# Kernel optimization log

Measured on AMD Instinct MI355X. Metric: run time of the kernel, lower is better.

The kernel has to match this reference:

```python
import jax, jax.numpy as jnp
import numpy as np
from math import factorial

# ---- module hyperparameters (from init_kwargs) ----
SPECIES = np.array([1, 6, 7, 8], np.int32)
LOW, HIGH, NG, RSWITCH, W, LMAX = 0.0, 6.0, 20, 1.0, 2.0, 2
LWEIGHTS = np.array([1.0, 1.0, 1.0], np.float32)
INVF = [2.0, 2.0, 2.0]


def _angular_tables():
    comps, weights, idx, inv = [], [], [], []
    for i in range(LMAX + 1):
        for k in range(i + 1):
            for m in range(i - k + 1):
                n = i - k - m
                comps.append([n, m, k])
                weights.append(factorial(i) / (factorial(n) * factorial(m) * factorial(k)))
                idx.append(i)
                inv.append(INVF[i])
    return (np.array(comps, np.int32), np.array(weights, np.float32),
            np.array(idx, np.int32), np.array(inv, np.float32))

COMPS, ANGW, ANGIDX, INVFACT = _angular_tables()   # 10 angular components for lmax=2
OFFSETS = np.linspace(LOW, HIGH, NG + 1, dtype=np.float32)[1:]
SQRTPI = np.float32(np.sqrt(np.pi))
NSP = len(SPECIES)
COMBOS = [(i, j) for i in range(NSP) for j in range(i + 1, NSP)]
NMBODY = NSP + len(COMBOS)
FPSIZE = NG * (LMAX + 1) * NMBODY


def _int_pow(x, e):
    # e in {0,1,2}; avoids NaN from pow(negative_base, float_exponent)
    return jnp.where(e == 0, jnp.ones_like(x), jnp.where(e == 1, x, x * x))


def _forward(coordinates, nuclear_charges, natom_counts, neighbours):
    B, N, _ = coordinates.shape
    mask = neighbours >= 0                              # padded slots are -1
    nb = jnp.maximum(neighbours, 0)                     # safe_fill
    bidx = jnp.arange(B)[:, None, None]
    local = coordinates[bidx, nb]                       # [B,N,M,3] neighbour gather
    nbh = coordinates[:, :, None, :] - local
    nbh = jnp.where(mask[..., None], nbh, 1.0)          # keep padded slots finite
    d = jnp.linalg.norm(nbh, axis=3)                    # [B,N,M]
    coeff = mask.astype(coordinates.dtype)
    nbr_z = nuclear_charges[bidx, nb]                   # [B,N,M]

    dsw = (d - RSWITCH) / (HIGH - RSWITCH)
    cut = 1.0 - 6.0 * dsw**5 + 15.0 * dsw**4 - 10.0 * dsw**3
    d2 = d * d
    sigma2 = jnp.log(1.0 + W / d2)
    mu = jnp.log(d / jnp.sqrt(1.0 + W / d2))
    off = jnp.asarray(OFFSETS)
    centered = (jnp.log(off) - mu[..., None]) ** 2      # [B,N,M,G]
    s2 = sigma2[..., None]
    radial = (1.0 / (off * jnp.sqrt(s2) * SQRTPI)) * jnp.exp(-centered / (2.0 * s2)) \
             * cut[..., None] * coeff[..., None]        # [B,N,M,G]

    expo = jnp.asarray(INVFACT + ANGIDX.astype(np.float32))
    inv_scaling = (1.0 / d[..., None]) ** expo * coeff[..., None]   # [B,N,M,A]
    comps = jnp.asarray(COMPS)
    angular = inv_scaling \
        * _int_pow(nbh[..., None, 0], comps[:, 0]) \
        * _int_pow(nbh[..., None, 1], comps[:, 1]) \
        * _int_pow(nbh[..., None, 2], comps[:, 2])      # [B,N,M,A]

    angw = jnp.asarray(ANGW)
    lw = jnp.asarray(LWEIGHTS)
    onehot = jnp.asarray((ANGIDX[:, None] == np.arange(LMAX + 1)[None, :]).astype(np.float32))

    sp_masks = [(nbr_z == int(z)).astype(coordinates.dtype) for z in SPECIES]

    def group_fp(gmask):
        ang = angular * gmask[..., None]
        t = jnp.einsum('bnma,bnmg->bnag', ang, radial)          # sum over neighbours
        orb = angw[None, None, :, None] * (t * t)               # [B,N,A,G]
        elem = jnp.einsum('bnag,al->bnlg', orb, onehot)         # index_add over l
        return lw[None, None, :, None] * elem                   # [B,N,L+1,G]

    fps = [group_fp(m) for m in sp_masks]
    for (i, j) in COMBOS:
        gmask = jnp.maximum(sp_masks[i], sp_masks[j])
        fps.append(group_fp(gmask) - (fps[i] + fps[j]))

    fp = jnp.stack(fps, axis=3)                                 # [B,N,L+1,NMBODY,G]
    atom_mask = (jnp.arange(N)[None, :] < natom_counts[:, None]).astype(coordinates.dtype)
    fp = fp * atom_mask[:, :, None, None, None]
    return fp.reshape(B, N, FPSIZE)


def setup_inputs() -> dict:
    rng = np.random.default_rng(0)
    B, N, M = 128, 128, 64
    box = 13.5
    coords = rng.uniform(0.0, box, (B, N, 3)).astype(np.float32)
    charges = rng.choice(np.array([1, 6, 7, 8], np.int32), size=(B, N)).astype(np.int32)
    counts = rng.integers(96, N + 1, B).astype(np.int32)
    diff = coords[:, :, None, :] - coords[:, None, :, :]
    dist = np.linalg.norm(diff, axis=-1)
    exist = np.arange(N)[None, :] < counts[:, None]
    valid = (dist < HIGH) & (dist > 1e-6) & exist[:, :, None] & exist[:, None, :]
    order = np.argsort(~valid, axis=2, kind='stable')[:, :, :M]
    vmask = np.take_along_axis(valid, order, axis=2)
    neighbours = np.where(vmask, order, -1).astype(np.int32)
    return {
        "coordinates": jnp.asarray(coords),
        "nuclear_charges": jnp.asarray(charges),
        "natom_counts": jnp.asarray(counts),
        "neighbours": jnp.asarray(neighbours),
    }


def reference(coordinates, nuclear_charges, natom_counts, neighbours):
    return _forward(coordinates, nuclear_charges, natom_counts, neighbours)
```

## Files before the change

### kernel.cpp

```cpp
#include <hip/hip_runtime.h>


#define B_   128
#define N_   128
#define M_   64
#define NG_  20
#define NSP_ 4
#define FPSIZE_ 600
#define APB  16
#define BLOCK_THREADS (APB * NG_)
#define NWAVE (BLOCK_THREADS / 64)
#define P1ITER ((APB + NWAVE - 1) / NWAVE)

__global__ __launch_bounds__(BLOCK_THREADS, 5)
void gto_fp_kernel(const float* __restrict__ coords,
                   const int*   __restrict__ charges,
                   const int*   __restrict__ counts,
                   const int*   __restrict__ neigh,
                   float*       __restrict__ out)
{
    __shared__ float4 sP[APB][M_ + 1];
    __shared__ float2 sQ[APB][M_ + 1];
    __shared__ int    s_seg[APB][NSP_ + 1];

    const int tid  = threadIdx.x;
    const int lane = tid & 63;
    const int wid  = tid >> 6;
    const int blockBase = blockIdx.x * APB;
    const int bidx = blockBase / N_;

#pragma unroll
    for (int it = 0; it < P1ITER; ++it) {
        const int la = wid + it * NWAVE;
        if (la < APB) {
            const int atom = blockBase + la;
            const int nb = neigh[atom * M_ + lane];
            bool v = (nb >= 0);
            int s = 0;
            float4 P = make_float4(0.f, 0.f, 0.f, 0.f);
            float2 Q = make_float2(0.f, 0.f);
            if (v) {
                const int nidx = bidx * N_ + nb;
                const float dx = coords[atom * 3 + 0] - coords[nidx * 3 + 0];
                const float dy = coords[atom * 3 + 1] - coords[nidx * 3 + 1];
                const float dz = coords[atom * 3 + 2] - coords[nidx * 3 + 2];
                const int   z  = charges[nidx];

                const float d2     = dx * dx + dy * dy + dz * dz;
                const float inv_d  = __builtin_amdgcn_rsqf(d2);
                const float d      = d2 * inv_d;
                const float inv_d2 = inv_d * inv_d;

                const float dsw  = (d - 1.0f) * 0.2f;
                const float dsw2 = dsw * dsw;
                const float cut  = 1.0f - dsw2 * dsw * fmaf(6.0f, dsw2, fmaf(-15.0f, dsw, 10.0f));

                const float sigma2 = __logf(fmaf(2.0f, inv_d2, 1.0f));
                const float mu     = 0.5f * (__logf(d2) - sigma2);
                const float amp    = fmaxf(__builtin_amdgcn_rsqf(sigma2) * cut * inv_d2,
                                           1.0e-30f);

                const float F  = -0.72134752f * __builtin_amdgcn_rcpf(sigma2);
                const float Fm = F * mu;
                const float c0 = F;
                const float c1 = -(Fm + Fm);
                const float c2 = fmaf(Fm, mu, __log2f(amp));

                s = (z == 1) ? 0 : (z - 5);
                P = make_float4(c0, c1, c2, dx * inv_d);
                Q = make_float2(dy * inv_d, dz * inv_d);
            }
            const unsigned long long b0 = __ballot(v && (s == 0));
            const unsigned long long b1 = __ballot(v && (s == 1));
            const unsigned long long b2 = __ballot(v && (s == 2));
            const unsigned long long b3 = __ballot(v && (s == 3));
            const int c0n = __popcll(b0), c1n = __popcll(b1),
                      c2n = __popcll(b2), c3n = __popcll(b3);
            const int o0 = __builtin_amdgcn_mbcnt_hi((unsigned)(b0 >> 32),
                           __builtin_amdgcn_mbcnt_lo((unsigned)b0, 0u));
            const int o1 = __builtin_amdgcn_mbcnt_hi((unsigned)(b1 >> 32),
                           __builtin_amdgcn_mbcnt_lo((unsigned)b1, 0u));
            const int o2 = __builtin_amdgcn_mbcnt_hi((unsigned)(b2 >> 32),
                           __builtin_amdgcn_mbcnt_lo((unsigned)b2, 0u));
            const int o3 = __builtin_amdgcn_mbcnt_hi((unsigned)(b3 >> 32),
                           __builtin_amdgcn_mbcnt_lo((unsigned)b3, 0u));
            int slot = o0;
            slot = (s == 1) ? c0n + o1 : slot;
            slot = (s == 2) ? c0n + c1n + o2 : slot;
            slot = (s == 3) ? c0n + c1n + c2n + o3 : slot;
            if (v) {
                sP[la][slot] = P;
                sQ[la][slot] = Q;
            }
            if (lane == 0) {
                s_seg[la][0] = 0;
                s_seg[la][1] = c0n;
                s_seg[la][2] = c0n + c1n;
                s_seg[la][3] = c0n + c1n + c2n;
                s_seg[la][4] = c0n + c1n + c2n + c3n;
            }
        }
    }
    __syncthreads();

    const int g  = tid % NG_;
    const int la = tid / NG_;
    const int atom = blockBase + la;
    const int n = atom % N_;

    const float off         = 0.3f * (float)(g + 1);
    const float lo          = __logf(off);
    const float lo2         = lo * lo;
    const float inv_off_spi = 1.0f / (off * 1.7724538509055159f);

    float T[NSP_][10];
#pragma unroll
    for (int s = 0; s < NSP_; ++s)
#pragma unroll
        for (int a = 0; a < 10; ++a) T[s][a] = 0.0f;

#define BODY(SS, P, Q)                                                        \
    {                                                                         \
        const float rad = __builtin_amdgcn_exp2f(                             \
            fmaf(P.x, lo2, fmaf(P.y, lo, P.z)));                              \
        const float rx = rad * P.w, ry = rad * Q.x, rz = rad * Q.y;           \
        T[SS][0] += rad;                                                      \
        T[SS][1] += rx;  T[SS][2] += ry;  T[SS][3] += rz;                     \
        T[SS][4] = fmaf(rx, P.w, T[SS][4]);                                   \
        T[SS][5] = fmaf(rx, Q.x, T[SS][5]);                                   \
        T[SS][6] = fmaf(ry, Q.x, T[SS][6]);                                   \
        T[SS][7] = fmaf(rx, Q.y, T[SS][7]);                                   \
        T[SS][8] = fmaf(ry, Q.y, T[SS][8]);                                   \
        T[SS][9] = fmaf(rz, Q.y, T[SS][9]);                                   \
    }

#define ACC(SS)                                                               \
    {                                                                         \
        const int e0 = s_seg[la][SS];                                         \
        const int e1 = s_seg[la][SS + 1];                                     \
        int m = e0;                                                           \
        for (; m + 3 < e1; m += 4) {                                          \
            const float4 Pa = sP[la][m];     const float2 Qa = sQ[la][m];     \
            const float4 Pb = sP[la][m + 1]; const float2 Qb = sQ[la][m + 1]; \
            const float4 Pc = sP[la][m + 2]; const float2 Qc = sQ[la][m + 2]; \
            const float4 Pd = sP[la][m + 3]; const float2 Qd = sQ[la][m + 3]; \
            BODY(SS, Pa, Qa)                                                  \
            BODY(SS, Pb, Qb)                                                  \
            BODY(SS, Pc, Qc)                                                  \
            BODY(SS, Pd, Qd)                                                  \
        }                                                                     \
        for (; m < e1; ++m) {                                                 \
            const float4 Pa = sP[la][m]; const float2 Qa = sQ[la][m];         \
            BODY(SS, Pa, Qa)                                                  \
        }                                                                     \
    }
    ACC(0) ACC(1) ACC(2) ACC(3)
#undef ACC
#undef BODY

    const float amask = (n < counts[bidx]) ? 1.0f : 0.0f;
    const float scale = amask * inv_off_spi * inv_off_spi;
    float* op = out + atom * FPSIZE_ + g;

#pragma unroll
    for (int l = 0; l < 3; ++l) {
        const int a0 = (l == 0) ? 0 : (l == 1) ? 1 : 4;
        const int a1 = (l == 0) ? 1 : (l == 1) ? 4 : 10;
#pragma unroll
        for (int s = 0; s < NSP_; ++s) {
            float v = 0.0f;
#pragma unroll
            for (int a = a0; a < a1; ++a) {
                const float w = (a == 5 || a == 7 || a == 8) ? 2.0f : 1.0f;
                v = fmaf(w * T[s][a], T[s][a], v);
            }
            op[(l * 10 + s) * NG_] = scale * v;
        }
        int mb = 4;
#pragma unroll
        for (int i = 0; i < NSP_; ++i) {
#pragma unroll
            for (int j = i + 1; j < NSP_; ++j) {
                float v = 0.0f;
#pragma unroll
                for (int a = a0; a < a1; ++a) {
                    const float w = (a == 5 || a == 7 || a == 8) ? 2.0f : 1.0f;
                    v = fmaf(w * T[i][a], T[j][a], v);
                }
                op[(l * 10 + mb) * NG_] = scale * (2.0f * v);
                ++mb;
            }
        }
    }
}

extern "C" void kernel_launch(void* const* d_in, const int* in_sizes, int n_in,
                              void* d_out, int out_size, void* d_ws, size_t ws_size,
                              hipStream_t stream) {
    const float* coords  = (const float*)d_in[0];
    const int*   charges = (const int*)d_in[1];
    const int*   counts  = (const int*)d_in[2];
    const int*   neigh   = (const int*)d_in[3];
    float*       outp    = (float*)d_out;

    const int blocks = (B_ * N_) / APB;
    gto_fp_kernel<<<blocks, BLOCK_THREADS, 0, stream>>>(coords, charges, counts, neigh, outp);
}
```

Before: 88.19 us.

## Compute two Gaussians per thread and stage molecule coords/charges in LDS

Each thread now handles two radial Gaussian offsets, g and g+10, instead of one. This halves the number of times each neighbour's P/Q entries are read from LDS and raises instruction-level parallelism. Blocks now cover 32 atoms with 10 threads each. The whole molecule's coordinates and species indices are first copied into shared memory, so the neighbour gather reads LDS instead of global memory. The costs are roughly double the accumulator registers (80 floats), more LDS per block, and dropping the occupancy hint from the launch bounds.

Result: no change. 88.48 us (+0.3%).

```diff
diff --git a/kernel.cpp b/kernel.cpp
--- a/kernel.cpp
+++ b/kernel.cpp
@@ -7,12 +7,13 @@
 #define NG_  20
 #define NSP_ 4
 #define FPSIZE_ 600
-#define APB  16
-#define BLOCK_THREADS (APB * NG_)
+#define APB  32
+#define TPA  10
+#define BLOCK_THREADS (APB * TPA)
 #define NWAVE (BLOCK_THREADS / 64)
 #define P1ITER ((APB + NWAVE - 1) / NWAVE)
 
-__global__ __launch_bounds__(BLOCK_THREADS, 5)
+__global__ __launch_bounds__(BLOCK_THREADS)
 void gto_fp_kernel(const float* __restrict__ coords,
                    const int*   __restrict__ charges,
                    const int*   __restrict__ counts,
@@ -21,30 +22,44 @@
 {
     __shared__ float4 sP[APB][M_ + 1];
     __shared__ float2 sQ[APB][M_ + 1];
+    __shared__ float  sC[3 * N_];
+    __shared__ int    sZ[N_];
     __shared__ int    s_seg[APB][NSP_ + 1];
 
     const int tid  = threadIdx.x;
     const int lane = tid & 63;
     const int wid  = tid >> 6;
     const int blockBase = blockIdx.x * APB;
-    const int bidx = blockBase / N_;
+    const int bidx      = blockBase / N_;
+    const int alocBase  = blockBase - bidx * N_;
+
+    for (int i = tid; i < 3 * N_; i += BLOCK_THREADS)
+        sC[i] = coords[bidx * 3 * N_ + i];
+    for (int i = tid; i < N_; i += BLOCK_THREADS) {
+        const int z = charges[bidx * N_ + i];
+        sZ[i] = (z == 1) ? 0 : (z - 5);
+    }
+    __syncthreads();
 
 #pragma unroll
     for (int it = 0; it < P1ITER; ++it) {
         const int la = wid + it * NWAVE;
         if (la < APB) {
             const int atom = blockBase + la;
+            const int aloc = alocBase + la;
             const int nb = neigh[atom * M_ + lane];
             bool v = (nb >= 0);
             int s = 0;
             float4 P = make_float4(0.f, 0.f, 0.f, 0.f);
             float2 Q = make_float2(0.f, 0.f);
             if (v) {
-                const int nidx = bidx * N_ + nb;
-                const float dx = coords[atom * 3 + 0] - coords[nidx * 3 + 0];
-                const float dy = coords[atom * 3 + 1] - coords[nidx * 3 + 1];
-                const float dz = coords[atom * 3 + 2] - coords[nidx * 3 + 2];
-                const int   z  = charges[nidx];
+                const float ax = sC[aloc * 3 + 0];
+                const float ay = sC[aloc * 3 + 1];
+                const float az = sC[aloc * 3 + 2];
+                const float dx = ax - sC[nb * 3 + 0];
+                const float dy = ay - sC[nb * 3 + 1];
+                const float dz = az - sC[nb * 3 + 2];
+                s = sZ[nb];
 
                 const float d2     = dx * dx + dy * dy + dz * dz;
                 const float inv_d  = __builtin_amdgcn_rsqf(d2);
@@ -66,7 +81,6 @@
                 const float c1 = -(Fm + Fm);
                 const float c2 = fmaf(Fm, mu, __log2f(amp));
 
-                s = (z == 1) ? 0 : (z - 5);
                 P = make_float4(c0, c1, c2, dx * inv_d);
                 Q = make_float2(dy * inv_d, dz * inv_d);
             }
@@ -103,35 +117,46 @@
     }
     __syncthreads();
 
-    const int g  = tid % NG_;
-    const int la = tid / NG_;
+    const int g0 = tid % TPA;
+    const int la = tid / TPA;
     const int atom = blockBase + la;
-    const int n = atom % N_;
-
-    const float off         = 0.3f * (float)(g + 1);
-    const float lo          = __logf(off);
-    const float lo2         = lo * lo;
-    const float inv_off_spi = 1.0f / (off * 1.7724538509055159f);
-
-    float T[NSP_][10];
+    const int aloc = alocBase + la;
+
+    const float offA = 0.3f * (float)(g0 + 1);
+    const float offB = 0.3f * (float)(g0 + 11);
+    const float loA = __logf(offA), loA2 = loA * loA;
+    const float loB = __logf(offB), loB2 = loB * loB;
+
+    float TA[NSP_][10], TB[NSP_][10];
 #pragma unroll
     for (int s = 0; s < NSP_; ++s)
 #pragma unroll
-        for (int a = 0; a < 10; ++a) T[s][a] = 0.0f;
+        for (int a = 0; a < 10; ++a) { TA[s][a] = 0.0f; TB[s][a] = 0.0f; }
 
 #define BODY(SS, P, Q)                                                        \
     {                                                                         \
-        const float rad = __builtin_amdgcn_exp2f(                             \
-            fmaf(P.x, lo2, fmaf(P.y, lo, P.z)));                              \
-        const float rx = rad * P.w, ry = rad * Q.x, rz = rad * Q.y;           \
-        T[SS][0] += rad;                                                      \
-        T[SS][1] += rx;  T[SS][2] += ry;  T[SS][3] += rz;                     \
-        T[SS][4] = fmaf(rx, P.w, T[SS][4]);                                   \
-        T[SS][5] = fmaf(rx, Q.x, T[SS][5]);                                   \
-        T[SS][6] = fmaf(ry, Q.x, T[SS][6]);                                   \
-        T[SS][7] = fmaf(rx, Q.y, T[SS][7]);                                   \
-        T[SS][8] = fmaf(ry, Q.y, T[SS][8]);                                   \
-        T[SS][9] = fmaf(rz, Q.y, T[SS][9]);                                   \
+        const float radA = __builtin_amdgcn_exp2f(                            \
+            fmaf(P.x, loA2, fmaf(P.y, loA, P.z)));                            \
+        const float radB = __builtin_amdgcn_exp2f(                            \
+            fmaf(P.x, loB2, fmaf(P.y, loB, P.z)));                            \
+        const float rxA = radA * P.w, ryA = radA * Q.x, rzA = radA * Q.y;     \
+        const float rxB = radB * P.w, ryB = radB * Q.x, rzB = radB * Q.y;     \
+        TA[SS][0] += radA;                 TB[SS][0] += radB;                 \
+        TA[SS][1] += rxA;                  TB[SS][1] += rxB;                  \
+        TA[SS][2] += ryA;                  TB[SS][2] += ryB;                  \
+        TA[SS][3] += rzA;                  TB[SS][3] += rzB;                  \
+        TA[SS][4] = fmaf(rxA, P.w, TA[SS][4]);                                \
+        TA[SS][5] = fmaf(rxA, Q.x, TA[SS][5]);                                \
+        TA[SS][6] = fmaf(ryA, Q.x, TA[SS][6]);                                \
+        TA[SS][7] = fmaf(rxA, Q.y, TA[SS][7]);                                \
+        TA[SS][8] = fmaf(ryA, Q.y, TA[SS][8]);                                \
+        TA[SS][9] = fmaf(rzA, Q.y, TA[SS][9]);                                \
+        TB[SS][4] = fmaf(rxB, P.w, TB[SS][4]);                                \
+        TB[SS][5] = fmaf(rxB, Q.x, TB[SS][5]);                                \
+        TB[SS][6] = fmaf(ryB, Q.x, TB[SS][6]);                                \
+        TB[SS][7] = fmaf(rxB, Q.y, TB[SS][7]);                                \
+        TB[SS][8] = fmaf(ryB, Q.y, TB[SS][8]);                                \
+        TB[SS][9] = fmaf(rzB, Q.y, TB[SS][9]);                                \
     }
 
 #define ACC(SS)                                                               \
@@ -139,17 +164,13 @@
         const int e0 = s_seg[la][SS];                                         \
         const int e1 = s_seg[la][SS + 1];                                     \
         int m = e0;                                                           \
-        for (; m + 3 < e1; m += 4) {                                          \
+        for (; m + 1 < e1; m += 2) {                                          \
             const float4 Pa = sP[la][m];     const float2 Qa = sQ[la][m];     \
             const float4 Pb = sP[la][m + 1]; const float2 Qb = sQ[la][m + 1]; \
-            const float4 Pc = sP[la][m + 2]; const float2 Qc = sQ[la][m + 2]; \
-            const float4 Pd = sP[la][m + 3]; const float2 Qd = sQ[la][m + 3]; \
             BODY(SS, Pa, Qa)                                                  \
             BODY(SS, Pb, Qb)                                                  \
-            BODY(SS, Pc, Qc)                                                  \
-            BODY(SS, Pd, Qd)                                                  \
         }                                                                     \
-        for (; m < e1; ++m) {                                                 \
+        if (m < e1) {                                                         \
             const float4 Pa = sP[la][m]; const float2 Qa = sQ[la][m];         \
             BODY(SS, Pa, Qa)                                                  \
         }                                                                     \
@@ -158,40 +179,45 @@
 #undef ACC
 #undef BODY
 
-    const float amask = (n < counts[bidx]) ? 1.0f : 0.0f;
-    const float scale = amask * inv_off_spi * inv_off_spi;
-    float* op = out + atom * FPSIZE_ + g;
-
-#pragma unroll
-    for (int l = 0; l < 3; ++l) {
-        const int a0 = (l == 0) ? 0 : (l == 1) ? 1 : 4;
-        const int a1 = (l == 0) ? 1 : (l == 1) ? 4 : 10;
-#pragma unroll
-        for (int s = 0; s < NSP_; ++s) {
-            float v = 0.0f;
-#pragma unroll
-            for (int a = a0; a < a1; ++a) {
-                const float w = (a == 5 || a == 7 || a == 8) ? 2.0f : 1.0f;
-                v = fmaf(w * T[s][a], T[s][a], v);
-            }
-            op[(l * 10 + s) * NG_] = scale * v;
-        }
-        int mb = 4;
-#pragma unroll
-        for (int i = 0; i < NSP_; ++i) {
-#pragma unroll
-            for (int j = i + 1; j < NSP_; ++j) {
+    const float amask = (aloc < counts[bidx]) ? 1.0f : 0.0f;
+
+    auto epilogue = [&](const float (&T)[NSP_][10], const int g, const float off) {
+        const float iosp  = 1.0f / (off * 1.7724538509055159f);
+        const float scale = amask * iosp * iosp;
+        float* op = out + atom * FPSIZE_ + g;
+#pragma unroll
+        for (int l = 0; l < 3; ++l) {
+            const int a0 = (l == 0) ? 0 : (l == 1) ? 1 : 4;
+            const int a1 = (l == 0) ? 1 : (l == 1) ? 4 : 10;
+#pragma unroll
+            for (int s = 0; s < NSP_; ++s) {
                 float v = 0.0f;
 #pragma unroll
                 for (int a = a0; a < a1; ++a) {
                     const float w = (a == 5 || a == 7 || a == 8) ? 2.0f : 1.0f;
-                    v = fmaf(w * T[i][a], T[j][a], v);
+                    v = fmaf(w * T[s][a], T[s][a], v);
                 }
-                op[(l * 10 + mb) * NG_] = scale * (2.0f * v);
-                ++mb;
+                op[(l * 10 + s) * NG_] = scale * v;
+            }
+            int mb = 4;
+#pragma unroll
+            for (int i = 0; i < NSP_; ++i) {
+#pragma unroll
+                for (int j = i + 1; j < NSP_; ++j) {
+                    float v = 0.0f;
+#pragma unroll
+                    for (int a = a0; a < a1; ++a) {
+                        const float w = (a == 5 || a == 7 || a == 8) ? 2.0f : 1.0f;
+                        v = fmaf(w * T[i][a], T[j][a], v);
+                    }
+                    op[(l * 10 + mb) * NG_] = scale * (2.0f * v);
+                    ++mb;
+                }
             }
         }
-    }
+    };
+    epilogue(TA, g0, offA);
+    epilogue(TB, g0 + 10, offB);
 }
 
 extern "C" void kernel_launch(void* const* d_in, const int* in_sizes, int n_in,
```

## Stage molecule coordinates in LDS, pair-store outputs, unroll tail, drop occupancy hint

Applied to the files above, without the earlier changes.

Each block now stages the whole molecule's coordinates and species indices into shared memory, so neighbour lookups read LDS instead of scattered global loads. Output stores are widened to float2 by exchanging values between adjacent lanes with a shuffle, so only even lanes write. The tail loop of the accumulation is unrolled into fixed 2+1 steps, and the min-blocks-per-CU launch bound is removed. This adds an extra barrier and LDS footprint per block, and the float2 stores rely on each lane pair sitting in the same wave and on 8-byte alignment.

After: 85.46 us. 3.1% less time.

```diff
diff --git a/kernel.cpp b/kernel.cpp
--- a/kernel.cpp
+++ b/kernel.cpp
@@ -8,11 +8,12 @@
 #define NSP_ 4
 #define FPSIZE_ 600
 #define APB  16
-#define BLOCK_THREADS (APB * NG_)
+#define TPA  20
+#define BLOCK_THREADS (APB * TPA)
 #define NWAVE (BLOCK_THREADS / 64)
 #define P1ITER ((APB + NWAVE - 1) / NWAVE)
 
-__global__ __launch_bounds__(BLOCK_THREADS, 5)
+__global__ __launch_bounds__(BLOCK_THREADS)
 void gto_fp_kernel(const float* __restrict__ coords,
                    const int*   __restrict__ charges,
                    const int*   __restrict__ counts,
@@ -21,30 +22,44 @@
 {
     __shared__ float4 sP[APB][M_ + 1];
     __shared__ float2 sQ[APB][M_ + 1];
+    __shared__ float  sC[3 * N_];
+    __shared__ int    sZ[N_];
     __shared__ int    s_seg[APB][NSP_ + 1];
 
     const int tid  = threadIdx.x;
     const int lane = tid & 63;
     const int wid  = tid >> 6;
     const int blockBase = blockIdx.x * APB;
-    const int bidx = blockBase / N_;
+    const int bidx      = blockBase / N_;
+    const int alocBase  = blockBase - bidx * N_;
+
+    for (int i = tid; i < 3 * N_; i += BLOCK_THREADS)
+        sC[i] = coords[bidx * 3 * N_ + i];
+    for (int i = tid; i < N_; i += BLOCK_THREADS) {
+        const int z = charges[bidx * N_ + i];
+        sZ[i] = (z == 1) ? 0 : (z - 5);
+    }
+    __syncthreads();
 
 #pragma unroll
     for (int it = 0; it < P1ITER; ++it) {
         const int la = wid + it * NWAVE;
         if (la < APB) {
             const int atom = blockBase + la;
+            const int aloc = alocBase + la;
             const int nb = neigh[atom * M_ + lane];
             bool v = (nb >= 0);
             int s = 0;
             float4 P = make_float4(0.f, 0.f, 0.f, 0.f);
             float2 Q = make_float2(0.f, 0.f);
             if (v) {
-                const int nidx = bidx * N_ + nb;
-                const float dx = coords[atom * 3 + 0] - coords[nidx * 3 + 0];
-                const float dy = coords[atom * 3 + 1] - coords[nidx * 3 + 1];
-                const float dz = coords[atom * 3 + 2] - coords[nidx * 3 + 2];
-                const int   z  = charges[nidx];
+                const float ax = sC[aloc * 3 + 0];
+                const float ay = sC[aloc * 3 + 1];
+                const float az = sC[aloc * 3 + 2];
+                const float dx = ax - sC[nb * 3 + 0];
+                const float dy = ay - sC[nb * 3 + 1];
+                const float dz = az - sC[nb * 3 + 2];
+                s = sZ[nb];
 
                 const float d2     = dx * dx + dy * dy + dz * dz;
                 const float inv_d  = __builtin_amdgcn_rsqf(d2);
@@ -66,7 +81,6 @@
                 const float c1 = -(Fm + Fm);
                 const float c2 = fmaf(Fm, mu, __log2f(amp));
 
-                s = (z == 1) ? 0 : (z - 5);
                 P = make_float4(c0, c1, c2, dx * inv_d);
                 Q = make_float2(dy * inv_d, dz * inv_d);
             }
@@ -103,15 +117,14 @@
     }
     __syncthreads();
 
-    const int g  = tid % NG_;
-    const int la = tid / NG_;
+    const int g  = tid % TPA;
+    const int la = tid / TPA;
     const int atom = blockBase + la;
-    const int n = atom % N_;
-
-    const float off         = 0.3f * (float)(g + 1);
-    const float lo          = __logf(off);
-    const float lo2         = lo * lo;
-    const float inv_off_spi = 1.0f / (off * 1.7724538509055159f);
+    const int aloc = alocBase + la;
+
+    const float off = 0.3f * (float)(g + 1);
+    const float lo  = __logf(off);
+    const float lo2 = lo * lo;
 
     float T[NSP_][10];
 #pragma unroll
@@ -149,7 +162,14 @@
             BODY(SS, Pc, Qc)                                                  \
             BODY(SS, Pd, Qd)                                                  \
         }                                                                     \
-        for (; m < e1; ++m) {                                                 \
+        if (m + 1 < e1) {                                                     \
+            const float4 Pa = sP[la][m];     const float2 Qa = sQ[la][m];     \
+            const float4 Pb = sP[la][m + 1]; const float2 Qb = sQ[la][m + 1]; \
+            BODY(SS, Pa, Qa)                                                  \
+            BODY(SS, Pb, Qb)                                                  \
+            m += 2;                                                           \
+        }                                                                     \
+        if (m < e1) {                                                         \
             const float4 Pa = sP[la][m]; const float2 Qa = sQ[la][m];         \
             BODY(SS, Pa, Qa)                                                  \
         }                                                                     \
@@ -158,9 +178,18 @@
 #undef ACC
 #undef BODY
 
-    const float amask = (n < counts[bidx]) ? 1.0f : 0.0f;
-    const float scale = amask * inv_off_spi * inv_off_spi;
+    const float amask = (aloc < counts[bidx]) ? 1.0f : 0.0f;
+    const float iosp  = 1.0f / (off * 1.7724538509055159f);
+    const float scale = amask * iosp * iosp;
+    const bool  geven = ((g & 1) == 0);
     float* op = out + atom * FPSIZE_ + g;
+
+#define EMIT(CH, V)                                                           \
+    {                                                                         \
+        const float _v  = (V);                                                \
+        const float _vp = __shfl_xor(_v, 1);                                  \
+        if (geven) *(float2*)(op + (CH) * NG_) = make_float2(_v, _vp);        \
+    }
 
 #pragma unroll
     for (int l = 0; l < 3; ++l) {
@@ -174,7 +203,7 @@
                 const float w = (a == 5 || a == 7 || a == 8) ? 2.0f : 1.0f;
                 v = fmaf(w * T[s][a], T[s][a], v);
             }
-            op[(l * 10 + s) * NG_] = scale * v;
+            EMIT(l * 10 + s, scale * v)
         }
         int mb = 4;
 #pragma unroll
@@ -187,11 +216,12 @@
                     const float w = (a == 5 || a == 7 || a == 8) ? 2.0f : 1.0f;
                     v = fmaf(w * T[i][a], T[j][a], v);
                 }
-                op[(l * 10 + mb) * NG_] = scale * (2.0f * v);
+                EMIT(l * 10 + mb, scale * (2.0f * v))
                 ++mb;
             }
         }
     }
+#undef EMIT
 }
 
 extern "C" void kernel_launch(void* const* d_in, const int* in_sizes, int n_in,
```
